# Kernel optimization log

Hardware: AMD Instinct MI355X
Metric: run time of the kernel (lower is better)

## Reference

```python
import math
import jax, jax.numpy as jnp
import numpy as np

NQ, NK = 4096, 8192
D_Q, D_K, D_ATTN, H, D_OUT = 256, 256, 64, 4, 256


def setup_inputs() -> dict:
    key = jax.random.key(0)
    ks = jax.random.split(key, 10)
    s = 0.02
    return {
        "x_Q": jax.random.normal(ks[0], (NQ, D_Q), jnp.float32),
        "x_K": jax.random.normal(ks[1], (NK, D_K), jnp.float32),
        "mask": jax.random.randint(ks[2], (NQ, NK), 0, 2, jnp.int32),
        # per-head projection weights, stored as (H, in, out) so y = x @ W
        "Wq": jax.random.normal(ks[3], (H, D_Q, D_ATTN), jnp.float32) * s,
        "Wk": jax.random.normal(ks[4], (H, D_K, D_ATTN), jnp.float32) * s,
        "Wv": jax.random.normal(ks[5], (H, D_K, D_ATTN), jnp.float32) * s,
        # per-head gate: Linear(d_Q, 1) + sigmoid
        "Wg": jax.random.normal(ks[6], (H, D_Q), jnp.float32) * s,
        "bg": jax.random.normal(ks[7], (H,), jnp.float32) * s,
        # output projection Linear(d_attn, d_out) with bias
        "Wo": jax.random.normal(ks[8], (D_ATTN, D_OUT), jnp.float32) * s,
        "bo": jax.random.normal(ks[9], (D_OUT,), jnp.float32) * s,
    }


def reference(x_Q, x_K, mask, Wq, Wk, Wv, Wg, bg, Wo, bo):
    m = mask.astype(x_Q.dtype)  # (NQ, NK) 0/1
    # Stacked per-head projections (original loops over heads)
    Q = jnp.einsum("nq,hqa->hna", x_Q, Wq)  # (H, NQ, A)
    K = jnp.einsum("mk,hka->hma", x_K, Wk)  # (H, NK, A)
    V = jnp.einsum("mk,hka->hma", x_K, Wv)  # (H, NK, A)
    scale = 1.0 / math.sqrt(D_ATTN)
    scores = jnp.einsum("hna,hma->hnm", Q, K) * scale  # (H, NQ, NK)
    # masked_softmax: (mask * x).masked_fill(mask == 0, -inf) then softmax over keys
    X = jnp.where(m == 0, -jnp.inf, m * scores)
    attn = jax.nn.softmax(X, axis=-1)
    heads = jnp.einsum("hnm,hma->hna", attn, V)  # (H, NQ, A)
    gates = jax.nn.sigmoid(jnp.einsum("nq,hq->hn", x_Q, Wg) + bg[:, None])  # (H, NQ)
    combined = jnp.einsum("hna,hn->na", heads, gates)  # (NQ, A)
    return combined @ Wo + bo  # (NQ, D_OUT)
```

## Files before the change

### kernel.cpp

```cpp
#include <hip/hip_runtime.h>
#include <hip/hip_bf16.h>

#define NQ 4096
#define NK 8192
#define DQK 256
#define DA 64
#define NH 4
#define DOUT 256
#define KSPLIT 16
#define KLEN (NK / KSPLIT)
#define NQT (NQ / 32)
#define NSUP 4
#define LOG2E 1.44269504088896340736f
#define QSCALE (0.125f * LOG2E)

typedef __attribute__((ext_vector_type(8))) short bf16x8;
typedef __attribute__((ext_vector_type(4))) float f32x4;
typedef __attribute__((ext_vector_type(4))) _Float16 f16x4;
typedef __attribute__((ext_vector_type(8))) _Float16 f16x8;

__device__ inline unsigned short f2bf(float f) {
  union { float f; unsigned u; } v; v.f = f;
  unsigned r = v.u + 0x7fff + ((v.u >> 16) & 1);
  return (unsigned short)(r >> 16);
}

__global__ __launch_bounds__(256) void maskbits_kernel(
    const int* __restrict__ mask, unsigned* __restrict__ bitsT) {
  const int NW = 8192 * 4;
  int wid = blockIdx.x * 4 + (threadIdx.x >> 6);
  int lane = threadIdx.x & 63;
  for (int j = 0; j < 2; ++j) {
    int v[8];
#pragma unroll
    for (int u = 0; u < 8; ++u) {
      int c = wid + (j * 8 + u) * NW;
      v[u] = mask[(size_t)(c >> 7) * NK + (c & 127) * 64 + lane];
    }
#pragma unroll
    for (int u = 0; u < 8; ++u) {
      unsigned long long b = __ballot(v[u] != 0);
      int c = wid + (j * 8 + u) * NW;
      int n = c >> 7, ch = c & 127;
      if (lane == 0)  bitsT[(size_t)(2 * ch) * NQ + n] = (unsigned)b;
      if (lane == 32) bitsT[(size_t)(2 * ch + 1) * NQ + n] = (unsigned)(b >> 32);
    }
  }
}

__global__ __launch_bounds__(256) void proj_kernel(
    const float* __restrict__ xQ, const float* __restrict__ xK,
    const float* __restrict__ Wq, const float* __restrict__ Wk,
    const float* __restrict__ Wv,
    unsigned short* __restrict__ Qp, unsigned short* __restrict__ Kp,
    _Float16* __restrict__ Vf) {
  __shared__ __align__(16) unsigned short Wt[64][264];

  int b = blockIdx.x;
  int proj, h, rb;
  if (b < 64)        { proj = 0; h = b >> 4;  rb = b & 15; }
  else if (b < 192)  { proj = 1; b -= 64;  h = b >> 5; rb = b & 31; }
  else               { proj = 2; b -= 192; h = b >> 5; rb = b & 31; }
  const float* x = (proj == 0) ? xQ : xK;
  const float* W = (proj == 0 ? Wq : (proj == 1 ? Wk : Wv)) + (size_t)h * 256 * 64;

  for (int i = threadIdx.x; i < 16384; i += 256)
    Wt[i & 63][i >> 6] = f2bf(W[i]);
  __syncthreads();

  int lane = threadIdx.x & 63, wv = threadIdx.x >> 6;
  int quad = lane >> 4, n16 = lane & 15;
  int r0 = rb * 256 + wv * 64;

  f32x4 acc[4][4];
#pragma unroll
  for (int mt = 0; mt < 4; ++mt)
#pragma unroll
    for (int nt = 0; nt < 4; ++nt)
      acc[mt][nt] = (f32x4){0.f, 0.f, 0.f, 0.f};

#pragma unroll
  for (int it = 0; it < 8; ++it) {
    const int k0 = it * 32;
    bf16x8 af[4];
#pragma unroll
    for (int mt = 0; mt < 4; ++mt) {
      const float* xp = x + (size_t)(r0 + mt * 16 + n16) * 256 + k0 + quad * 8;
      const float4 a0 = *(const float4*)xp;
      const float4 a1 = *(const float4*)(xp + 4);
      bf16x8 a;
      a[0] = (short)f2bf(a0.x); a[1] = (short)f2bf(a0.y);
      a[2] = (short)f2bf(a0.z); a[3] = (short)f2bf(a0.w);
      a[4] = (short)f2bf(a1.x); a[5] = (short)f2bf(a1.y);
      a[6] = (short)f2bf(a1.z); a[7] = (short)f2bf(a1.w);
      af[mt] = a;
    }
    bf16x8 bfr[4];
#pragma unroll
    for (int nt = 0; nt < 4; ++nt)
      bfr[nt] = *(const bf16x8*)&Wt[nt * 16 + n16][k0 + quad * 8];
#pragma unroll
    for (int mt = 0; mt < 4; ++mt)
#pragma unroll
      for (int nt = 0; nt < 4; ++nt)
        acc[mt][nt] = __builtin_amdgcn_mfma_f32_16x16x32_bf16(
            af[mt], bfr[nt], acc[mt][nt], 0, 0, 0);
  }

  if (proj < 2) {
    unsigned short* outp =
        (proj == 0 ? Qp : Kp) + (size_t)h * (size_t)(proj == 0 ? NQ : NK) * 64;
    const float sc = (proj == 0) ? QSCALE : 1.0f;
#pragma unroll
    for (int mt = 0; mt < 4; ++mt)
#pragma unroll
      for (int nt = 0; nt < 4; ++nt)
#pragma unroll
        for (int r = 0; r < 4; ++r) {
          int row = r0 + mt * 16 + quad * 4 + r;
          int col = nt * 16 + n16;
          outp[(size_t)row * 64 + col] = f2bf(acc[mt][nt][r] * sc);
        }
  } else {
#pragma unroll
    for (int mt = 0; mt < 4; ++mt) {
      int tile = h * 256 + ((r0 + mt * 16) >> 5);
      int kr = mt & 1;
#pragma unroll
      for (int nt = 0; nt < 4; ++nt) {
        f16x4 pk;
        pk[0] = (_Float16)acc[mt][nt][0]; pk[1] = (_Float16)acc[mt][nt][1];
        pk[2] = (_Float16)acc[mt][nt][2]; pk[3] = (_Float16)acc[mt][nt][3];
        *(f16x4*)&Vf[(((size_t)tile * 8 + kr * 4 + nt) * 64 + lane) * 4] = pk;
      }
    }
  }
}

__global__ __launch_bounds__(256, 4) void attn_kernel(
    const unsigned short* __restrict__ Qp, const unsigned short* __restrict__ Kp,
    const _Float16* __restrict__ Vf, const unsigned* __restrict__ bitsT,
    _Float16* __restrict__ Opart, float* __restrict__ Lpart) {
  __shared__ __align__(16) float Ob[32][68];
  __shared__ float Lb[32];

  int b = blockIdx.x;
  int ksg = b & 3, h = (b >> 2) & 3, qt = b >> 4;
  int wv = threadIdx.x >> 6, lane = threadIdx.x & 63;
  int quad = lane >> 4, n16 = lane & 15;
  int ks = ksg * 4 + wv;
  int qb = qt * 32;

  bf16x8 qf[2][2];
#pragma unroll
  for (int qc = 0; qc < 2; ++qc)
#pragma unroll
    for (int c = 0; c < 2; ++c)
      qf[qc][c] = *(const bf16x8*)&Qp[((size_t)h * NQ + qb + qc * 16 + n16) * 64 +
                                      c * 32 + quad * 8];

  f32x4 o[4][2];
#pragma unroll
  for (int dt = 0; dt < 4; ++dt)
#pragma unroll
    for (int qc = 0; qc < 2; ++qc) o[dt][qc] = (f32x4){0.f, 0.f, 0.f, 0.f};
  float ls[2] = {0.f, 0.f};

  const unsigned short* Kptr =
      Kp + (size_t)h * NK * 64 + (size_t)(ks * KLEN + n16) * 64 + quad * 8;
  const _Float16* Vbase = Vf + ((size_t)h * 256 + ks * 16) * 2048 + lane * 4;
  const unsigned* bT = bitsT + (size_t)(ks * 16) * NQ + qb;

#pragma unroll 2
  for (int kb = 0; kb < KLEN / 32; ++kb) {
    unsigned wqa0 = bT[(size_t)kb * NQ + n16];
    unsigned wqa1 = bT[(size_t)kb * NQ + 16 + n16];

    const unsigned short* Kg = Kptr + (size_t)kb * 32 * 64;
    bf16x8 kf[2][2];
#pragma unroll
    for (int kr = 0; kr < 2; ++kr)
#pragma unroll
      for (int c = 0; c < 2; ++c)
        kf[kr][c] = *(const bf16x8*)(Kg + kr * 16 * 64 + c * 32);

    const _Float16* Vg = Vbase + (size_t)kb * 2048;
    f16x4 vf[4][2];
#pragma unroll
    for (int kr = 0; kr < 2; ++kr)
#pragma unroll
      for (int dt = 0; dt < 4; ++dt)
        vf[dt][kr] = *(const f16x4*)(Vg + (kr * 4 + dt) * 256);

    f32x4 s[2][2];
#pragma unroll
    for (int kr = 0; kr < 2; ++kr)
#pragma unroll
      for (int qc = 0; qc < 2; ++qc) {
        f32x4 acc = (f32x4){0.f, 0.f, 0.f, 0.f};
        acc = __builtin_amdgcn_mfma_f32_16x16x32_bf16(kf[kr][0], qf[qc][0], acc, 0, 0, 0);
        acc = __builtin_amdgcn_mfma_f32_16x16x32_bf16(kf[kr][1], qf[qc][1], acc, 0, 0, 0);
        s[kr][qc] = acc;
      }

#pragma unroll
    for (int qc = 0; qc < 2; ++qc) {
      unsigned wq = (qc == 0 ? wqa0 : wqa1) >> (quad * 4);
      f16x4 pf[2];
#pragma unroll
      for (int kr = 0; kr < 2; ++kr) {
        float e0 = __builtin_amdgcn_exp2f(s[kr][qc][0]);
        float e1 = __builtin_amdgcn_exp2f(s[kr][qc][1]);
        float e2 = __builtin_amdgcn_exp2f(s[kr][qc][2]);
        float e3 = __builtin_amdgcn_exp2f(s[kr][qc][3]);
        e0 = (wq & (1u << (kr * 16 + 0))) ? e0 : 0.f;
        e1 = (wq & (1u << (kr * 16 + 1))) ? e1 : 0.f;
        e2 = (wq & (1u << (kr * 16 + 2))) ? e2 : 0.f;
        e3 = (wq & (1u << (kr * 16 + 3))) ? e3 : 0.f;
        ls[qc] += (e0 + e1) + (e2 + e3);
        f16x4 p;
        p[0] = (_Float16)e0; p[1] = (_Float16)e1;
        p[2] = (_Float16)e2; p[3] = (_Float16)e3;
        pf[kr] = p;
      }
#pragma unroll
      for (int dt = 0; dt < 4; ++dt) {
        o[dt][qc] = __builtin_amdgcn_mfma_f32_16x16x16f16(vf[dt][0], pf[0],
                                                          o[dt][qc], 0, 0, 0);
        o[dt][qc] = __builtin_amdgcn_mfma_f32_16x16x16f16(vf[dt][1], pf[1],
                                                          o[dt][qc], 0, 0, 0);
      }
    }
  }

#pragma unroll
  for (int qc = 0; qc < 2; ++qc) {
    ls[qc] += __shfl_xor(ls[qc], 16);
    ls[qc] += __shfl_xor(ls[qc], 32);
  }

#pragma unroll
  for (int w = 0; w < 4; ++w) {
    if (wv == w) {
      if (w == 0) {
#pragma unroll
        for (int qc = 0; qc < 2; ++qc)
#pragma unroll
          for (int dt = 0; dt < 4; ++dt)
            *(f32x4*)&Ob[qc * 16 + n16][dt * 16 + quad * 4] = o[dt][qc];
        if (quad == 0) { Lb[n16] = ls[0]; Lb[16 + n16] = ls[1]; }
      } else {
#pragma unroll
        for (int qc = 0; qc < 2; ++qc)
#pragma unroll
          for (int dt = 0; dt < 4; ++dt) {
            f32x4 t = *(f32x4*)&Ob[qc * 16 + n16][dt * 16 + quad * 4];
            t += o[dt][qc];
            *(f32x4*)&Ob[qc * 16 + n16][dt * 16 + quad * 4] = t;
          }
        if (quad == 0) { Lb[n16] += ls[0]; Lb[16 + n16] += ls[1]; }
      }
    }
    __syncthreads();
  }

  const size_t tile = ((size_t)h * NQT + qt) * NSUP + ksg;
  {
    int tid = threadIdx.x;
    int r = tid >> 3, c0 = (tid & 7) * 8;
    f32x4 a = *(f32x4*)&Ob[r][c0];
    f32x4 b2 = *(f32x4*)&Ob[r][c0 + 4];
    f16x8 ov;
    ov[0] = (_Float16)a[0]; ov[1] = (_Float16)a[1];
    ov[2] = (_Float16)a[2]; ov[3] = (_Float16)a[3];
    ov[4] = (_Float16)b2[0]; ov[5] = (_Float16)b2[1];
    ov[6] = (_Float16)b2[2]; ov[7] = (_Float16)b2[3];
    *(f16x8*)&Opart[(tile * 32 + r) * 64 + c0] = ov;
    if (tid < 32) Lpart[tile * 32 + tid] = Lb[tid];
  }
}

__global__ __launch_bounds__(256) void combine_kernel(
    const _Float16* __restrict__ Opart, const float* __restrict__ Lpart,
    const float* __restrict__ xQ, const float* __restrict__ Wg,
    const float* __restrict__ bg, const float* __restrict__ Wo,
    const float* __restrict__ bo, float* __restrict__ out) {
  __shared__ float comb[16][64];
  __shared__ float gred[16][4][4];
  __shared__ float glds[16][4];
  int nb = blockIdx.x;
  int tid = threadIdx.x;

  {
    int r = tid >> 4, hh = (tid >> 2) & 3, c = tid & 3;
    const float* xp = xQ + (size_t)(nb * 16 + r) * 256 + c * 64;
    const float* wp = Wg + hh * 256 + c * 64;
    float s = 0.f;
#pragma unroll
    for (int e = 0; e < 64; ++e) s = fmaf(xp[e], wp[e], s);
    gred[r][hh][c] = s;
  }
  __syncthreads();
  if (tid < 64) {
    int r = tid >> 2, hh = tid & 3;
    float s = gred[r][hh][0] + gred[r][hh][1] + gred[r][hh][2] + gred[r][hh][3];
    glds[r][hh] = 1.f / (1.f + __expf(-(s + bg[hh])));
  }
  __syncthreads();

  int r4 = tid >> 6, a = tid & 63;
  int qt = nb >> 1, rbase = (nb & 1) * 16;

  for (int p = 0; p < 4; ++p) {
    int r = p * 4 + r4;
    int rl = rbase + r;
    float csum = 0.f;
#pragma unroll
    for (int h = 0; h < NH; ++h) {
      size_t t0 = ((size_t)h * NQT + qt) * NSUP;
      float accO = 0.f, lt = 0.f;
#pragma unroll
      for (int s = 0; s < NSUP; ++s) {
        size_t t = t0 + s;
        accO += (float)Opart[(t * 32 + rl) * 64 + a];
        lt += Lpart[t * 32 + rl];
      }
      csum += glds[r][h] * accO / lt;
    }
    comb[r][a] = csum;
  }
  __syncthreads();

  int j = tid;
  float accv[16];
#pragma unroll
  for (int r = 0; r < 16; ++r) accv[r] = bo[j];
  for (int aa = 0; aa < 64; ++aa) {
    float w = Wo[(size_t)aa * 256 + j];
#pragma unroll
    for (int r = 0; r < 16; ++r) accv[r] = fmaf(comb[r][aa], w, accv[r]);
  }
#pragma unroll
  for (int r = 0; r < 16; ++r)
    out[(size_t)(nb * 16 + r) * 256 + j] = accv[r];
}

extern "C" void kernel_launch(void* const* d_in, const int* in_sizes, int n_in,
                              void* d_out, int out_size, void* d_ws, size_t ws_size,
                              hipStream_t stream) {
  const float* xQ  = (const float*)d_in[0];
  const float* xK  = (const float*)d_in[1];
  const int*   mask= (const int*)d_in[2];
  const float* Wq  = (const float*)d_in[3];
  const float* Wk  = (const float*)d_in[4];
  const float* Wv  = (const float*)d_in[5];
  const float* Wg  = (const float*)d_in[6];
  const float* bg  = (const float*)d_in[7];
  const float* Wo  = (const float*)d_in[8];
  const float* bo  = (const float*)d_in[9];
  float* out = (float*)d_out;

  char* ws = (char*)d_ws;
  unsigned short* Qp   = (unsigned short*)(ws + 0);
  unsigned short* Kp   = (unsigned short*)(ws + 2097152);
  _Float16*       Vfp  = (_Float16*)(ws + 6291456);
  unsigned*       bitsT= (unsigned*)(ws + 10485760);
  float*          Lp   = (float*)(ws + 14680064);
  _Float16*       Op   = (_Float16*)(ws + 14942208);

  maskbits_kernel<<<dim3(8192), dim3(256), 0, stream>>>(mask, bitsT);
  proj_kernel<<<dim3(320), dim3(256), 0, stream>>>(xQ, xK, Wq, Wk, Wv, Qp, Kp, Vfp);
  attn_kernel<<<dim3(2048), dim3(256), 0, stream>>>(Qp, Kp, Vfp, bitsT, Op, Lp);
  combine_kernel<<<dim3(NQ / 16), dim3(256), 0, stream>>>(Op, Lp, xQ, Wg, bg,
                                                          Wo, bo, out);
}
```

Measured before the change: 358.2 us.

## Merge mask and projection kernels; remap attention waves to separate query tiles

The mask bit-packing and QKV projection kernels are merged into one launch, with block ranges dispatched by block index, which removes a kernel boundary. In the attention kernel, each wave now handles a different query tile for the same key split instead of different key splits for the same queries. This removes the LDS reduction across waves and its four barriers, and each wave writes its fp16 partial outputs directly. In exchange, the number of partials per query rises from 4 to 16, so the combine kernel reads four times as much partial data. Waves in a block also no longer share K/V/mask data through cache in the same way.

```diff
diff --git a/kernel.cpp b/kernel.cpp
--- a/kernel.cpp
+++ b/kernel.cpp
@@ -10,14 +10,12 @@
 #define KSPLIT 16
 #define KLEN (NK / KSPLIT)
 #define NQT (NQ / 32)
-#define NSUP 4
 #define LOG2E 1.44269504088896340736f
 #define QSCALE (0.125f * LOG2E)
 
 typedef __attribute__((ext_vector_type(8))) short bf16x8;
 typedef __attribute__((ext_vector_type(4))) float f32x4;
 typedef __attribute__((ext_vector_type(4))) _Float16 f16x4;
-typedef __attribute__((ext_vector_type(8))) _Float16 f16x8;
 
 __device__ inline unsigned short f2bf(float f) {
   union { float f; unsigned u; } v; v.f = f;
@@ -25,30 +23,8 @@
   return (unsigned short)(r >> 16);
 }
 
-__global__ __launch_bounds__(256) void maskbits_kernel(
-    const int* __restrict__ mask, unsigned* __restrict__ bitsT) {
-  const int NW = 8192 * 4;
-  int wid = blockIdx.x * 4 + (threadIdx.x >> 6);
-  int lane = threadIdx.x & 63;
-  for (int j = 0; j < 2; ++j) {
-    int v[8];
-#pragma unroll
-    for (int u = 0; u < 8; ++u) {
-      int c = wid + (j * 8 + u) * NW;
-      v[u] = mask[(size_t)(c >> 7) * NK + (c & 127) * 64 + lane];
-    }
-#pragma unroll
-    for (int u = 0; u < 8; ++u) {
-      unsigned long long b = __ballot(v[u] != 0);
-      int c = wid + (j * 8 + u) * NW;
-      int n = c >> 7, ch = c & 127;
-      if (lane == 0)  bitsT[(size_t)(2 * ch) * NQ + n] = (unsigned)b;
-      if (lane == 32) bitsT[(size_t)(2 * ch + 1) * NQ + n] = (unsigned)(b >> 32);
-    }
-  }
-}
-
-__global__ __launch_bounds__(256) void proj_kernel(
+__global__ __launch_bounds__(256) void prep_kernel(
+    const int* __restrict__ mask, unsigned* __restrict__ bitsT,
     const float* __restrict__ xQ, const float* __restrict__ xK,
     const float* __restrict__ Wq, const float* __restrict__ Wk,
     const float* __restrict__ Wv,
@@ -56,7 +32,30 @@
     _Float16* __restrict__ Vf) {
   __shared__ __align__(16) unsigned short Wt[64][264];
 
-  int b = blockIdx.x;
+  if (blockIdx.x < 8192) {
+    const int NW = 8192 * 4;
+    int wid = blockIdx.x * 4 + (threadIdx.x >> 6);
+    int lane = threadIdx.x & 63;
+    for (int j = 0; j < 2; ++j) {
+      int v[8];
+#pragma unroll
+      for (int u = 0; u < 8; ++u) {
+        int c = wid + (j * 8 + u) * NW;
+        v[u] = mask[(size_t)(c >> 7) * NK + (c & 127) * 64 + lane];
+      }
+#pragma unroll
+      for (int u = 0; u < 8; ++u) {
+        unsigned long long b = __ballot(v[u] != 0);
+        int c = wid + (j * 8 + u) * NW;
+        int n = c >> 7, ch = c & 127;
+        if (lane == 0)  bitsT[(size_t)(2 * ch) * NQ + n] = (unsigned)b;
+        if (lane == 32) bitsT[(size_t)(2 * ch + 1) * NQ + n] = (unsigned)(b >> 32);
+      }
+    }
+    return;
+  }
+
+  int b = blockIdx.x - 8192;
   int proj, h, rb;
   if (b < 64)        { proj = 0; h = b >> 4;  rb = b & 15; }
   else if (b < 192)  { proj = 1; b -= 64;  h = b >> 5; rb = b & 31; }
@@ -141,14 +140,11 @@
     const unsigned short* __restrict__ Qp, const unsigned short* __restrict__ Kp,
     const _Float16* __restrict__ Vf, const unsigned* __restrict__ bitsT,
     _Float16* __restrict__ Opart, float* __restrict__ Lpart) {
-  __shared__ __align__(16) float Ob[32][68];
-  __shared__ float Lb[32];
-
   int b = blockIdx.x;
-  int ksg = b & 3, h = (b >> 2) & 3, qt = b >> 4;
+  int qg = b & 31, ks = (b >> 5) & 15, h = b >> 9;
   int wv = threadIdx.x >> 6, lane = threadIdx.x & 63;
   int quad = lane >> 4, n16 = lane & 15;
-  int ks = ksg * 4 + wv;
+  int qt = qg * 4 + wv;
   int qb = qt * 32;
 
   bf16x8 qf[2][2];
@@ -239,44 +235,21 @@
     ls[qc] += __shfl_xor(ls[qc], 32);
   }
 
-#pragma unroll
-  for (int w = 0; w < 4; ++w) {
-    if (wv == w) {
-      if (w == 0) {
-#pragma unroll
-        for (int qc = 0; qc < 2; ++qc)
-#pragma unroll
-          for (int dt = 0; dt < 4; ++dt)
-            *(f32x4*)&Ob[qc * 16 + n16][dt * 16 + quad * 4] = o[dt][qc];
-        if (quad == 0) { Lb[n16] = ls[0]; Lb[16 + n16] = ls[1]; }
-      } else {
-#pragma unroll
-        for (int qc = 0; qc < 2; ++qc)
-#pragma unroll
-          for (int dt = 0; dt < 4; ++dt) {
-            f32x4 t = *(f32x4*)&Ob[qc * 16 + n16][dt * 16 + quad * 4];
-            t += o[dt][qc];
-            *(f32x4*)&Ob[qc * 16 + n16][dt * 16 + quad * 4] = t;
-          }
-        if (quad == 0) { Lb[n16] += ls[0]; Lb[16 + n16] += ls[1]; }
-      }
-    }
-    __syncthreads();
-  }
-
-  const size_t tile = ((size_t)h * NQT + qt) * NSUP + ksg;
-  {
-    int tid = threadIdx.x;
-    int r = tid >> 3, c0 = (tid & 7) * 8;
-    f32x4 a = *(f32x4*)&Ob[r][c0];
-    f32x4 b2 = *(f32x4*)&Ob[r][c0 + 4];
-    f16x8 ov;
-    ov[0] = (_Float16)a[0]; ov[1] = (_Float16)a[1];
-    ov[2] = (_Float16)a[2]; ov[3] = (_Float16)a[3];
-    ov[4] = (_Float16)b2[0]; ov[5] = (_Float16)b2[1];
-    ov[6] = (_Float16)b2[2]; ov[7] = (_Float16)b2[3];
-    *(f16x8*)&Opart[(tile * 32 + r) * 64 + c0] = ov;
-    if (tid < 32) Lpart[tile * 32 + tid] = Lb[tid];
+  const size_t tile = ((size_t)h * NQT + qt) * KSPLIT + ks;
+#pragma unroll
+  for (int qc = 0; qc < 2; ++qc) {
+#pragma unroll
+    for (int dt = 0; dt < 4; ++dt) {
+      size_t idx = (tile * 32 + qc * 16 + n16) * 64 + dt * 16 + quad * 4;
+      f16x4 ov;
+      ov[0] = (_Float16)o[dt][qc][0]; ov[1] = (_Float16)o[dt][qc][1];
+      ov[2] = (_Float16)o[dt][qc][2]; ov[3] = (_Float16)o[dt][qc][3];
+      *(f16x4*)&Opart[idx] = ov;
+    }
+  }
+  if (quad == 0) {
+    Lpart[tile * 32 + n16] = ls[0];
+    Lpart[tile * 32 + 16 + n16] = ls[1];
   }
 }
 
@@ -317,10 +290,10 @@
     float csum = 0.f;
 #pragma unroll
     for (int h = 0; h < NH; ++h) {
-      size_t t0 = ((size_t)h * NQT + qt) * NSUP;
+      size_t t0 = ((size_t)h * NQT + qt) * KSPLIT;
       float accO = 0.f, lt = 0.f;
 #pragma unroll
-      for (int s = 0; s < NSUP; ++s) {
+      for (int s = 0; s < KSPLIT; ++s) {
         size_t t = t0 + s;
         accO += (float)Opart[(t * 32 + rl) * 64 + a];
         lt += Lpart[t * 32 + rl];
@@ -366,10 +339,10 @@
   _Float16*       Vfp  = (_Float16*)(ws + 6291456);
   unsigned*       bitsT= (unsigned*)(ws + 10485760);
   float*          Lp   = (float*)(ws + 14680064);
-  _Float16*       Op   = (_Float16*)(ws + 14942208);
-
-  maskbits_kernel<<<dim3(8192), dim3(256), 0, stream>>>(mask, bitsT);
-  proj_kernel<<<dim3(320), dim3(256), 0, stream>>>(xQ, xK, Wq, Wk, Wv, Qp, Kp, Vfp);
+  _Float16*       Op   = (_Float16*)(ws + 15728640);
+
+  prep_kernel<<<dim3(8512), dim3(256), 0, stream>>>(
+      mask, bitsT, xQ, xK, Wq, Wk, Wv, Qp, Kp, Vfp);
   attn_kernel<<<dim3(2048), dim3(256), 0, stream>>>(Qp, Kp, Vfp, bitsT, Op, Lp);
   combine_kernel<<<dim3(NQ / 16), dim3(256), 0, stream>>>(Op, Lp, xQ, Wg, bg,
                                                           Wo, bo, out);
```

Measured after the change: 418.4 us. 16.8% more time.

## Widen attention query tile to 64 rows to reuse K/V loads

Applied to the files above, without the earlier changes.

Each attention block now covers 64 query rows instead of 32, so every K and V fragment loaded from global memory feeds four query chunks rather than two. The grid is halved and the head index moves to the high block bits. Q fragments are now reloaded from global/L2 inside the key loop rather than kept in registers, which keeps register pressure down but adds repeated Q traffic. Shared-memory buffers, the partial-output layout, the workspace offset and the combine indexing are all updated to match the 64-row tiles.

```diff
diff --git a/kernel.cpp b/kernel.cpp
--- a/kernel.cpp
+++ b/kernel.cpp
@@ -3,21 +3,16 @@
 
 #define NQ 4096
 #define NK 8192
-#define DQK 256
-#define DA 64
 #define NH 4
-#define DOUT 256
 #define KSPLIT 16
 #define KLEN (NK / KSPLIT)
-#define NQT (NQ / 32)
+#define NQT64 (NQ / 64)
 #define NSUP 4
-#define LOG2E 1.44269504088896340736f
-#define QSCALE (0.125f * LOG2E)
+#define QSCALE (0.125f * 1.44269504088896340736f)
 
 typedef __attribute__((ext_vector_type(8))) short bf16x8;
 typedef __attribute__((ext_vector_type(4))) float f32x4;
 typedef __attribute__((ext_vector_type(4))) _Float16 f16x4;
-typedef __attribute__((ext_vector_type(8))) _Float16 f16x8;
 
 __device__ inline unsigned short f2bf(float f) {
   union { float f; unsigned u; } v; v.f = f;
@@ -141,31 +136,24 @@
     const unsigned short* __restrict__ Qp, const unsigned short* __restrict__ Kp,
     const _Float16* __restrict__ Vf, const unsigned* __restrict__ bitsT,
     _Float16* __restrict__ Opart, float* __restrict__ Lpart) {
-  __shared__ __align__(16) float Ob[32][68];
-  __shared__ float Lb[32];
+  __shared__ __align__(16) float Ob[64][68];
+  __shared__ float Lb[64];
 
   int b = blockIdx.x;
-  int ksg = b & 3, h = (b >> 2) & 3, qt = b >> 4;
+  int ksg = b & 3, qt64 = (b >> 2) & 63, h = b >> 8;
   int wv = threadIdx.x >> 6, lane = threadIdx.x & 63;
   int quad = lane >> 4, n16 = lane & 15;
   int ks = ksg * 4 + wv;
-  int qb = qt * 32;
-
-  bf16x8 qf[2][2];
-#pragma unroll
-  for (int qc = 0; qc < 2; ++qc)
-#pragma unroll
-    for (int c = 0; c < 2; ++c)
-      qf[qc][c] = *(const bf16x8*)&Qp[((size_t)h * NQ + qb + qc * 16 + n16) * 64 +
-                                      c * 32 + quad * 8];
-
-  f32x4 o[4][2];
+  int qb = qt64 * 64;
+
+  f32x4 o[4][4];
 #pragma unroll
   for (int dt = 0; dt < 4; ++dt)
 #pragma unroll
-    for (int qc = 0; qc < 2; ++qc) o[dt][qc] = (f32x4){0.f, 0.f, 0.f, 0.f};
-  float ls[2] = {0.f, 0.f};
-
+    for (int qc = 0; qc < 4; ++qc) o[dt][qc] = (f32x4){0.f, 0.f, 0.f, 0.f};
+  float ls[4] = {0.f, 0.f, 0.f, 0.f};
+
+  const unsigned short* Qbase = Qp + ((size_t)h * NQ + qb) * 64;
   const unsigned short* Kptr =
       Kp + (size_t)h * NK * 64 + (size_t)(ks * KLEN + n16) * 64 + quad * 8;
   const _Float16* Vbase = Vf + ((size_t)h * 256 + ks * 16) * 2048 + lane * 4;
@@ -173,9 +161,6 @@
 
 #pragma unroll 2
   for (int kb = 0; kb < KLEN / 32; ++kb) {
-    unsigned wqa0 = bT[(size_t)kb * NQ + n16];
-    unsigned wqa1 = bT[(size_t)kb * NQ + 16 + n16];
-
     const unsigned short* Kg = Kptr + (size_t)kb * 32 * 64;
     bf16x8 kf[2][2];
 #pragma unroll
@@ -192,27 +177,29 @@
       for (int dt = 0; dt < 4; ++dt)
         vf[dt][kr] = *(const f16x4*)(Vg + (kr * 4 + dt) * 256);
 
-    f32x4 s[2][2];
-#pragma unroll
-    for (int kr = 0; kr < 2; ++kr)
-#pragma unroll
-      for (int qc = 0; qc < 2; ++qc) {
-        f32x4 acc = (f32x4){0.f, 0.f, 0.f, 0.f};
-        acc = __builtin_amdgcn_mfma_f32_16x16x32_bf16(kf[kr][0], qf[qc][0], acc, 0, 0, 0);
-        acc = __builtin_amdgcn_mfma_f32_16x16x32_bf16(kf[kr][1], qf[qc][1], acc, 0, 0, 0);
-        s[kr][qc] = acc;
-      }
-
-#pragma unroll
-    for (int qc = 0; qc < 2; ++qc) {
-      unsigned wq = (qc == 0 ? wqa0 : wqa1) >> (quad * 4);
+#pragma unroll
+    for (int qc = 0; qc < 4; ++qc) {
+      bf16x8 q0 = *(const bf16x8*)&Qbase[(size_t)(qc * 16 + n16) * 64 + quad * 8];
+      bf16x8 q1 = *(const bf16x8*)&Qbase[(size_t)(qc * 16 + n16) * 64 + 32 + quad * 8];
+      unsigned wqa = bT[(size_t)kb * NQ + qc * 16 + n16];
+
+      f32x4 s[2];
+#pragma unroll
+      for (int kr = 0; kr < 2; ++kr) {
+        f32x4 a2 = (f32x4){0.f, 0.f, 0.f, 0.f};
+        a2 = __builtin_amdgcn_mfma_f32_16x16x32_bf16(kf[kr][0], q0, a2, 0, 0, 0);
+        a2 = __builtin_amdgcn_mfma_f32_16x16x32_bf16(kf[kr][1], q1, a2, 0, 0, 0);
+        s[kr] = a2;
+      }
+
+      unsigned wq = wqa >> (quad * 4);
       f16x4 pf[2];
 #pragma unroll
       for (int kr = 0; kr < 2; ++kr) {
-        float e0 = __builtin_amdgcn_exp2f(s[kr][qc][0]);
-        float e1 = __builtin_amdgcn_exp2f(s[kr][qc][1]);
-        float e2 = __builtin_amdgcn_exp2f(s[kr][qc][2]);
-        float e3 = __builtin_amdgcn_exp2f(s[kr][qc][3]);
+        float e0 = __builtin_amdgcn_exp2f(s[kr][0]);
+        float e1 = __builtin_amdgcn_exp2f(s[kr][1]);
+        float e2 = __builtin_amdgcn_exp2f(s[kr][2]);
+        float e3 = __builtin_amdgcn_exp2f(s[kr][3]);
         e0 = (wq & (1u << (kr * 16 + 0))) ? e0 : 0.f;
         e1 = (wq & (1u << (kr * 16 + 1))) ? e1 : 0.f;
         e2 = (wq & (1u << (kr * 16 + 2))) ? e2 : 0.f;
@@ -234,7 +221,7 @@
   }
 
 #pragma unroll
-  for (int qc = 0; qc < 2; ++qc) {
+  for (int qc = 0; qc < 4; ++qc) {
     ls[qc] += __shfl_xor(ls[qc], 16);
     ls[qc] += __shfl_xor(ls[qc], 32);
   }
@@ -244,39 +231,41 @@
     if (wv == w) {
       if (w == 0) {
 #pragma unroll
-        for (int qc = 0; qc < 2; ++qc)
+        for (int qc = 0; qc < 4; ++qc) {
 #pragma unroll
           for (int dt = 0; dt < 4; ++dt)
             *(f32x4*)&Ob[qc * 16 + n16][dt * 16 + quad * 4] = o[dt][qc];
-        if (quad == 0) { Lb[n16] = ls[0]; Lb[16 + n16] = ls[1]; }
+          if (quad == 0) Lb[qc * 16 + n16] = ls[qc];
+        }
       } else {
 #pragma unroll
-        for (int qc = 0; qc < 2; ++qc)
+        for (int qc = 0; qc < 4; ++qc) {
 #pragma unroll
           for (int dt = 0; dt < 4; ++dt) {
             f32x4 t = *(f32x4*)&Ob[qc * 16 + n16][dt * 16 + quad * 4];
             t += o[dt][qc];
             *(f32x4*)&Ob[qc * 16 + n16][dt * 16 + quad * 4] = t;
           }
-        if (quad == 0) { Lb[n16] += ls[0]; Lb[16 + n16] += ls[1]; }
+          if (quad == 0) Lb[qc * 16 + n16] += ls[qc];
+        }
       }
     }
     __syncthreads();
   }
 
-  const size_t tile = ((size_t)h * NQT + qt) * NSUP + ksg;
+  const size_t tile = ((size_t)h * NQT64 + qt64) * NSUP + ksg;
   {
     int tid = threadIdx.x;
-    int r = tid >> 3, c0 = (tid & 7) * 8;
-    f32x4 a = *(f32x4*)&Ob[r][c0];
-    f32x4 b2 = *(f32x4*)&Ob[r][c0 + 4];
-    f16x8 ov;
-    ov[0] = (_Float16)a[0]; ov[1] = (_Float16)a[1];
-    ov[2] = (_Float16)a[2]; ov[3] = (_Float16)a[3];
-    ov[4] = (_Float16)b2[0]; ov[5] = (_Float16)b2[1];
-    ov[6] = (_Float16)b2[2]; ov[7] = (_Float16)b2[3];
-    *(f16x8*)&Opart[(tile * 32 + r) * 64 + c0] = ov;
-    if (tid < 32) Lpart[tile * 32 + tid] = Lb[tid];
+    int r = tid >> 2, c0 = (tid & 3) * 16;
+#pragma unroll
+    for (int g = 0; g < 4; ++g) {
+      f32x4 a = *(f32x4*)&Ob[r][c0 + g * 4];
+      f16x4 ov;
+      ov[0] = (_Float16)a[0]; ov[1] = (_Float16)a[1];
+      ov[2] = (_Float16)a[2]; ov[3] = (_Float16)a[3];
+      *(f16x4*)&Opart[(tile * 64 + r) * 64 + c0 + g * 4] = ov;
+    }
+    if (tid < 64) Lpart[tile * 64 + tid] = Lb[tid];
   }
 }
 
@@ -309,21 +298,21 @@
   __syncthreads();
 
   int r4 = tid >> 6, a = tid & 63;
-  int qt = nb >> 1, rbase = (nb & 1) * 16;
 
   for (int p = 0; p < 4; ++p) {
     int r = p * 4 + r4;
-    int rl = rbase + r;
+    int n = nb * 16 + r;
+    int qt64 = n >> 6, rl = n & 63;
     float csum = 0.f;
 #pragma unroll
     for (int h = 0; h < NH; ++h) {
-      size_t t0 = ((size_t)h * NQT + qt) * NSUP;
+      size_t t0 = ((size_t)h * NQT64 + qt64) * NSUP;
       float accO = 0.f, lt = 0.f;
 #pragma unroll
       for (int s = 0; s < NSUP; ++s) {
         size_t t = t0 + s;
-        accO += (float)Opart[(t * 32 + rl) * 64 + a];
-        lt += Lpart[t * 32 + rl];
+        accO += (float)Opart[(t * 64 + rl) * 64 + a];
+        lt += Lpart[t * 64 + rl];
       }
       csum += glds[r][h] * accO / lt;
     }
@@ -366,11 +355,11 @@
   _Float16*       Vfp  = (_Float16*)(ws + 6291456);
   unsigned*       bitsT= (unsigned*)(ws + 10485760);
   float*          Lp   = (float*)(ws + 14680064);
-  _Float16*       Op   = (_Float16*)(ws + 14942208);
+  _Float16*       Op   = (_Float16*)(ws + 15728640);
 
   maskbits_kernel<<<dim3(8192), dim3(256), 0, stream>>>(mask, bitsT);
   proj_kernel<<<dim3(320), dim3(256), 0, stream>>>(xQ, xK, Wq, Wk, Wv, Qp, Kp, Vfp);
-  attn_kernel<<<dim3(2048), dim3(256), 0, stream>>>(Qp, Kp, Vfp, bitsT, Op, Lp);
+  attn_kernel<<<dim3(1024), dim3(256), 0, stream>>>(Qp, Kp, Vfp, bitsT, Op, Lp);
   combine_kernel<<<dim3(NQ / 16), dim3(256), 0, stream>>>(Op, Lp, xQ, Wg, bg,
                                                           Wo, bo, out);
 }
```

Result: slower. 477.1 us (+33.2%).
